# Performance work log

Hardware: AMD Instinct MI355X
Metric: run time of the kernel (lower is better)

Reference implementation:

```python
import jax, jax.numpy as jnp
import numpy as np

NUM_EMBEDDINGS = 512
EMBEDDING_DIM = 64
DECAY = 0.995
EXPECTED_COUNT = 1024 * 16 * 16 / NUM_EMBEDDINGS  # batch_size * H * W / K = 512.0


def setup_inputs() -> dict:
    key = jax.random.key(0)
    k1, k2 = jax.random.split(key)
    z_e = jax.random.normal(k1, (1024, EMBEDDING_DIM, 16, 16), dtype=jnp.float32)
    e = jax.random.normal(k2, (NUM_EMBEDDINGS, EMBEDDING_DIM), dtype=jnp.float32)
    N = jnp.ones((NUM_EMBEDDINGS,), dtype=jnp.float32) * EXPECTED_COUNT
    return {"z_e": z_e, "e": e, "N": N}


def reference(z_e, e, N):
    B, D, H, W = z_e.shape
    # (B, D, H, W) -> (B*H*W, D)
    z_flat = jnp.transpose(z_e, (0, 2, 3, 1)).reshape(-1, D)
    # squared euclidean distances: ||z||^2 + ||e||^2 - 2 z.e^T  -> [B*H*W, K]
    dist = (
        jnp.sum(z_flat * z_flat, axis=1, keepdims=True)
        + jnp.sum(e * e, axis=1)[None, :]
        - 2.0 * (z_flat @ e.T)
    )
    indices_flat = jnp.argmin(dist, axis=1)
    # embedding gather, back to (B, D, H, W)
    z_q = e[indices_flat].reshape(B, H, W, D)
    z_q = jnp.transpose(z_q, (0, 3, 1, 2))
    # training-mode EMA bincount update of cluster counts
    n_i = jnp.zeros((e.shape[0],), dtype=jnp.float32).at[indices_flat].add(1.0)
    N_new = DECAY * N + (1.0 - DECAY) * n_i
    return z_q, N_new
```

## Files before the change

kernel.cpp:

```cpp
#include <hip/hip_runtime.h>

#define KCODES 512
#define DIM    64
#define PXB    512
#define NCT    32

typedef __attribute__((ext_vector_type(8))) short  short8;
typedef __attribute__((ext_vector_type(4))) float  floatx4;

__device__ inline unsigned short f2bf(float x) {
    unsigned u = __float_as_uint(x);
    return (unsigned short)((u + 0x7FFFu + ((u >> 16) & 1u)) >> 16);
}
__device__ inline float bf2f(unsigned short h) { return __uint_as_float(((unsigned)h) << 16); }

__global__ __launch_bounds__(256) void vq_setup(const float* __restrict__ e,
        float* __restrict__ enorm, unsigned short* __restrict__ ehs,
        unsigned short* __restrict__ els, float* __restrict__ counts,
        unsigned* __restrict__ tick)
{
    const int tg = blockIdx.x * 256 + threadIdx.x;
    const int c = tg >> 6, j = tg & 63;
    const int p = j >> 3, i = j & 7;
    const int dsrc = ((p ^ (c & 7)) << 3) | i;
    float x = -2.f * e[c * DIM + dsrc];
    unsigned short h = f2bf(x);
    ehs[tg] = h;
    els[tg] = f2bf(x - bf2f(h));
    if (tg < KCODES) {
        const float* er = e + tg * DIM;
        float s = 0.f;
        #pragma unroll
        for (int d = 0; d < DIM; ++d) s = fmaf(er[d], er[d], s);
        enorm[tg]  = s;
        counts[tg] = 0.f;
        if (tg == 0) *tick = 0u;
    }
}

__global__ __launch_bounds__(1024) void vq_main(
        const float* __restrict__ z, const float* __restrict__ e,
        const unsigned short* __restrict__ ehs, const unsigned short* __restrict__ els,
        const float* __restrict__ enorm, const float* __restrict__ N,
        float* __restrict__ zq, float* __restrict__ counts,
        unsigned* __restrict__ tick, float* __restrict__ outN)
{
    __shared__ __align__(16) unsigned short eHs[KCODES * DIM];
    __shared__ __align__(16) unsigned short eLs[KCODES * DIM];
    __shared__ float ens[KCODES];
    __shared__ int   hist[KCODES];
    __shared__ int   idxs[PXB];
    __shared__ int   lastflag;

    const int t    = threadIdx.x;
    const int b    = blockIdx.x;
    const int lane = t & 63;
    const int wave = t >> 6;
    const int n16  = lane & 15;
    const int g4   = lane >> 4;

    {
        const short8* sh = (const short8*)ehs;
        const short8* sl = (const short8*)els;
        short8* dh = (short8*)eHs;
        short8* dl = (short8*)eLs;
        #pragma unroll
        for (int k = 0; k < 4; ++k) {
            dh[t + k * 1024] = sh[t + k * 1024];
            dl[t + k * 1024] = sl[t + k * 1024];
        }
        if (t < KCODES) { ens[t] = enorm[t]; hist[t] = 0; }
    }

    const int gp0 = b * PXB + wave * 32;
    short8 Ah[2][2], Al[2][2];
    #pragma unroll
    for (int pt = 0; pt < 2; ++pt) {
        const int gp = gp0 + pt * 16 + n16;
        const int bb = gp >> 8, hw = gp & 255;
        const float* zb = z + (size_t)bb * (DIM * 256) + hw;
        #pragma unroll
        for (int ks = 0; ks < 2; ++ks) {
            float v[8];
            #pragma unroll
            for (int q = 0; q < 8; ++q)
                v[q] = zb[(size_t)(ks * 32 + g4 * 8 + q) * 256];
            short8 hi, lo;
            #pragma unroll
            for (int q = 0; q < 8; ++q) {
                unsigned short h = f2bf(v[q]);
                hi[q] = (short)h;
                lo[q] = (short)f2bf(v[q] - bf2f(h));
            }
            Ah[pt][ks] = hi; Al[pt][ks] = lo;
        }
    }

    __syncthreads();

    const int xr = n16 & 7;
    const int byte_ks0 = n16 * 128 + (((g4    ) ^ xr) << 4);
    const int byte_ks1 = n16 * 128 + (((4 | g4) ^ xr) << 4);
    const char* hb = (const char*)eHs;
    const char* lb = (const char*)eLs;

    float bestv[2][4];
    int   bct[2][4];
    #pragma unroll
    for (int pt = 0; pt < 2; ++pt)
        #pragma unroll
        for (int r = 0; r < 4; ++r) { bestv[pt][r] = 3.4e38f; bct[pt][r] = 0; }

    #pragma unroll 4
    for (int ct = 0; ct < NCT; ++ct) {
        const int cb = ct * 2048;
        short8 Bh0 = *(const short8*)(hb + cb + byte_ks0);
        short8 Bh1 = *(const short8*)(hb + cb + byte_ks1);
        short8 Bl0 = *(const short8*)(lb + cb + byte_ks0);
        short8 Bl1 = *(const short8*)(lb + cb + byte_ks1);
        const float en = ens[ct * 16 + n16];
        #pragma unroll
        for (int pt = 0; pt < 2; ++pt) {
            floatx4 C = {en, en, en, en};
            C = __builtin_amdgcn_mfma_f32_16x16x32_bf16(Ah[pt][0], Bl0, C, 0, 0, 0);
            C = __builtin_amdgcn_mfma_f32_16x16x32_bf16(Ah[pt][1], Bl1, C, 0, 0, 0);
            C = __builtin_amdgcn_mfma_f32_16x16x32_bf16(Al[pt][0], Bh0, C, 0, 0, 0);
            C = __builtin_amdgcn_mfma_f32_16x16x32_bf16(Al[pt][1], Bh1, C, 0, 0, 0);
            C = __builtin_amdgcn_mfma_f32_16x16x32_bf16(Ah[pt][0], Bh0, C, 0, 0, 0);
            C = __builtin_amdgcn_mfma_f32_16x16x32_bf16(Ah[pt][1], Bh1, C, 0, 0, 0);
            #pragma unroll
            for (int r = 0; r < 4; ++r) {
                float s = C[r];
                if (s < bestv[pt][r]) { bestv[pt][r] = s; bct[pt][r] = ct; }
            }
        }
    }

    #pragma unroll
    for (int pt = 0; pt < 2; ++pt)
        #pragma unroll
        for (int r = 0; r < 4; ++r) {
            float v  = bestv[pt][r];
            int   id = bct[pt][r] * 16 + n16;
            #pragma unroll
            for (int off = 1; off < 16; off <<= 1) {
                float v1 = __shfl_xor(v, off, 16);
                int   i1 = __shfl_xor(id, off, 16);
                if (v1 < v || (v1 == v && i1 < id)) { v = v1; id = i1; }
            }
            if (n16 == 0) {
                const int px = wave * 32 + pt * 16 + g4 * 4 + r;
                idxs[px] = id;
                atomicAdd(&hist[id], 1);
            }
        }

    __syncthreads();

    {
        const int px = t & 511, dh = (t >> 9) * 32;
        const int bi = idxs[px];
        const int gp = b * PXB + px;
        const int bb = gp >> 8, hw = gp & 255;
        const float4* er4 = (const float4*)(e + bi * DIM + dh);
        float* ob = zq + (size_t)bb * (DIM * 256) + (size_t)dh * 256 + hw;
        #pragma unroll
        for (int q = 0; q < 8; ++q) {
            float4 v = er4[q];
            ob[(size_t)(4 * q + 0) * 256] = v.x;
            ob[(size_t)(4 * q + 1) * 256] = v.y;
            ob[(size_t)(4 * q + 2) * 256] = v.z;
            ob[(size_t)(4 * q + 3) * 256] = v.w;
        }
    }

    if (t < KCODES) { int h = hist[t]; if (h) atomicAdd(&counts[t], (float)h); }

    __syncthreads();
    if (t == 0) {
        __threadfence();
        unsigned o = __hip_atomic_fetch_add(tick, 1u, __ATOMIC_ACQ_REL,
                                            __HIP_MEMORY_SCOPE_AGENT);
        lastflag = (o == gridDim.x - 1u);
    }
    __syncthreads();
    if (lastflag && t < KCODES) {
        float c = __hip_atomic_load(&counts[t], __ATOMIC_RELAXED,
                                    __HIP_MEMORY_SCOPE_AGENT);
        outN[t] = 0.995f * N[t] + 0.005f * c;
    }
}

extern "C" void kernel_launch(void* const* d_in, const int* in_sizes, int n_in,
                              void* d_out, int out_size, void* d_ws, size_t ws_size,
                              hipStream_t stream) {
    const float* z = (const float*)d_in[0];
    const float* e = (const float*)d_in[1];
    const float* N = (const float*)d_in[2];
    float* out = (float*)d_out;
    const int nz     = in_sizes[0];
    const int npix   = nz / DIM;
    const int blocks = npix / PXB;

    char* ws = (char*)d_ws;
    float*          enorm  = (float*)(ws);
    float*          counts = (float*)(ws + 2048);
    unsigned*       tick   = (unsigned*)(ws + 4096);
    unsigned short* ehs    = (unsigned short*)(ws + 4352);
    unsigned short* els    = (unsigned short*)(ws + 4352 + KCODES * DIM * 2);

    vq_setup<<<(KCODES * DIM) / 256, 256, 0, stream>>>(e, enorm, ehs, els, counts, tick);
    vq_main<<<blocks, 1024, 0, stream>>>(z, e, ehs, els, enorm, N, out, counts,
                                         tick, out + nz);
}
```

Baseline: 202.2 us.

## Use single-pass fp16 MFMA distances with fp32 refinement of near-tie candidates

Replaces the split bf16 hi/lo three-product MFMA scheme with a single fp16 MFMA pass, which cuts the MFMA count per tile from six to two and halves LDS codebook traffic and footprint. A second shuffle reduction tracks the runner-up code. When the runner-up is within a fixed margin of the best, the pixel's two candidates are rescored exactly in fp32 from global memory. The histogram and count-flush ordering are moved to after this refinement. The risk is argmin mismatches if fp16 error exceeds the margin, plus extra work in the refinement pass.

```diff
diff --git a/kernel.cpp b/kernel.cpp
--- a/kernel.cpp
+++ b/kernel.cpp
@@ -4,29 +4,21 @@
 #define DIM    64
 #define PXB    512
 #define NCT    32
-
-typedef __attribute__((ext_vector_type(8))) short  short8;
-typedef __attribute__((ext_vector_type(4))) float  floatx4;
-
-__device__ inline unsigned short f2bf(float x) {
-    unsigned u = __float_as_uint(x);
-    return (unsigned short)((u + 0x7FFFu + ((u >> 16) & 1u)) >> 16);
-}
-__device__ inline float bf2f(unsigned short h) { return __uint_as_float(((unsigned)h) << 16); }
+#define MARGIN 0.125f
+
+typedef __attribute__((ext_vector_type(8))) short    short8;
+typedef __attribute__((ext_vector_type(8))) _Float16 half8;
+typedef __attribute__((ext_vector_type(4))) float    floatx4;
 
 __global__ __launch_bounds__(256) void vq_setup(const float* __restrict__ e,
-        float* __restrict__ enorm, unsigned short* __restrict__ ehs,
-        unsigned short* __restrict__ els, float* __restrict__ counts,
-        unsigned* __restrict__ tick)
+        float* __restrict__ enorm, _Float16* __restrict__ ehf,
+        float* __restrict__ counts, unsigned* __restrict__ tick)
 {
     const int tg = blockIdx.x * 256 + threadIdx.x;
     const int c = tg >> 6, j = tg & 63;
     const int p = j >> 3, i = j & 7;
     const int dsrc = ((p ^ (c & 7)) << 3) | i;
-    float x = -2.f * e[c * DIM + dsrc];
-    unsigned short h = f2bf(x);
-    ehs[tg] = h;
-    els[tg] = f2bf(x - bf2f(h));
+    ehf[tg] = (_Float16)(-2.f * e[c * DIM + dsrc]);
     if (tg < KCODES) {
         const float* er = e + tg * DIM;
         float s = 0.f;
@@ -38,18 +30,18 @@
     }
 }
 
-__global__ __launch_bounds__(1024) void vq_main(
+__global__ __launch_bounds__(1024, 8) void vq_main(
         const float* __restrict__ z, const float* __restrict__ e,
-        const unsigned short* __restrict__ ehs, const unsigned short* __restrict__ els,
-        const float* __restrict__ enorm, const float* __restrict__ N,
-        float* __restrict__ zq, float* __restrict__ counts,
-        unsigned* __restrict__ tick, float* __restrict__ outN)
+        const _Float16* __restrict__ ehf, const float* __restrict__ enorm,
+        const float* __restrict__ N, float* __restrict__ zq,
+        float* __restrict__ counts, unsigned* __restrict__ tick,
+        float* __restrict__ outN)
 {
-    __shared__ __align__(16) unsigned short eHs[KCODES * DIM];
-    __shared__ __align__(16) unsigned short eLs[KCODES * DIM];
+    __shared__ __align__(16) _Float16 eHs[KCODES * DIM];
     __shared__ float ens[KCODES];
     __shared__ int   hist[KCODES];
     __shared__ int   idxs[PXB];
+    __shared__ int   ref2[PXB];
     __shared__ int   lastflag;
 
     const int t    = threadIdx.x;
@@ -60,20 +52,16 @@
     const int g4   = lane >> 4;
 
     {
-        const short8* sh = (const short8*)ehs;
-        const short8* sl = (const short8*)els;
-        short8* dh = (short8*)eHs;
-        short8* dl = (short8*)eLs;
-        #pragma unroll
-        for (int k = 0; k < 4; ++k) {
-            dh[t + k * 1024] = sh[t + k * 1024];
-            dl[t + k * 1024] = sl[t + k * 1024];
-        }
+        const short8* src = (const short8*)ehf;
+        short8* dst = (short8*)eHs;
+        #pragma unroll
+        for (int k = 0; k < 4; ++k)
+            dst[t + k * 1024] = src[t + k * 1024];
         if (t < KCODES) { ens[t] = enorm[t]; hist[t] = 0; }
     }
 
     const int gp0 = b * PXB + wave * 32;
-    short8 Ah[2][2], Al[2][2];
+    half8 A[2][2];
     #pragma unroll
     for (int pt = 0; pt < 2; ++pt) {
         const int gp = gp0 + pt * 16 + n16;
@@ -85,24 +73,19 @@
             #pragma unroll
             for (int q = 0; q < 8; ++q)
                 v[q] = zb[(size_t)(ks * 32 + g4 * 8 + q) * 256];
-            short8 hi, lo;
-            #pragma unroll
-            for (int q = 0; q < 8; ++q) {
-                unsigned short h = f2bf(v[q]);
-                hi[q] = (short)h;
-                lo[q] = (short)f2bf(v[q] - bf2f(h));
-            }
-            Ah[pt][ks] = hi; Al[pt][ks] = lo;
+            half8 h;
+            #pragma unroll
+            for (int q = 0; q < 8; ++q) h[q] = (_Float16)v[q];
+            A[pt][ks] = h;
         }
     }
 
     __syncthreads();
 
     const int xr = n16 & 7;
-    const int byte_ks0 = n16 * 128 + (((g4    ) ^ xr) << 4);
-    const int byte_ks1 = n16 * 128 + (((4 | g4) ^ xr) << 4);
+    const int byte0 = n16 * 128 + (((g4    ) ^ xr) << 4);
+    const int byte1 = n16 * 128 + (((4 | g4) ^ xr) << 4);
     const char* hb = (const char*)eHs;
-    const char* lb = (const char*)eLs;
 
     float bestv[2][4];
     int   bct[2][4];
@@ -111,23 +94,17 @@
         #pragma unroll
         for (int r = 0; r < 4; ++r) { bestv[pt][r] = 3.4e38f; bct[pt][r] = 0; }
 
-    #pragma unroll 4
+    #pragma unroll 2
     for (int ct = 0; ct < NCT; ++ct) {
         const int cb = ct * 2048;
-        short8 Bh0 = *(const short8*)(hb + cb + byte_ks0);
-        short8 Bh1 = *(const short8*)(hb + cb + byte_ks1);
-        short8 Bl0 = *(const short8*)(lb + cb + byte_ks0);
-        short8 Bl1 = *(const short8*)(lb + cb + byte_ks1);
+        half8 B0 = *(const half8*)(hb + cb + byte0);
+        half8 B1 = *(const half8*)(hb + cb + byte1);
         const float en = ens[ct * 16 + n16];
         #pragma unroll
         for (int pt = 0; pt < 2; ++pt) {
             floatx4 C = {en, en, en, en};
-            C = __builtin_amdgcn_mfma_f32_16x16x32_bf16(Ah[pt][0], Bl0, C, 0, 0, 0);
-            C = __builtin_amdgcn_mfma_f32_16x16x32_bf16(Ah[pt][1], Bl1, C, 0, 0, 0);
-            C = __builtin_amdgcn_mfma_f32_16x16x32_bf16(Al[pt][0], Bh0, C, 0, 0, 0);
-            C = __builtin_amdgcn_mfma_f32_16x16x32_bf16(Al[pt][1], Bh1, C, 0, 0, 0);
-            C = __builtin_amdgcn_mfma_f32_16x16x32_bf16(Ah[pt][0], Bh0, C, 0, 0, 0);
-            C = __builtin_amdgcn_mfma_f32_16x16x32_bf16(Ah[pt][1], Bh1, C, 0, 0, 0);
+            C = __builtin_amdgcn_mfma_f32_16x16x32_f16(A[pt][0], B0, C, 0, 0, 0);
+            C = __builtin_amdgcn_mfma_f32_16x16x32_f16(A[pt][1], B1, C, 0, 0, 0);
             #pragma unroll
             for (int r = 0; r < 4; ++r) {
                 float s = C[r];
@@ -140,21 +117,66 @@
     for (int pt = 0; pt < 2; ++pt)
         #pragma unroll
         for (int r = 0; r < 4; ++r) {
-            float v  = bestv[pt][r];
-            int   id = bct[pt][r] * 16 + n16;
+            const float v1 = bestv[pt][r];
+            const int   i1 = bct[pt][r] * 16 + n16;
+            float v = v1; int i = i1;
             #pragma unroll
             for (int off = 1; off < 16; off <<= 1) {
-                float v1 = __shfl_xor(v, off, 16);
-                int   i1 = __shfl_xor(id, off, 16);
-                if (v1 < v || (v1 == v && i1 < id)) { v = v1; id = i1; }
+                float vs = __shfl_xor(v, off, 16);
+                int   is = __shfl_xor(i, off, 16);
+                if (vs < v || (vs == v && is < i)) { v = vs; i = is; }
+            }
+            float w  = (i1 == i) ? 3.4e38f : v1;
+            int   wi = i1;
+            #pragma unroll
+            for (int off = 1; off < 16; off <<= 1) {
+                float vs = __shfl_xor(w, off, 16);
+                int   is = __shfl_xor(wi, off, 16);
+                if (vs < w || (vs == w && is < wi)) { w = vs; wi = is; }
             }
             if (n16 == 0) {
                 const int px = wave * 32 + pt * 16 + g4 * 4 + r;
-                idxs[px] = id;
-                atomicAdd(&hist[id], 1);
-            }
-        }
-
+                idxs[px] = i;
+                ref2[px] = (w - v < MARGIN) ? wi : -1;
+            }
+        }
+
+    __syncthreads();
+
+    if (t < PXB) {
+        int bi = idxs[t];
+        const int r2 = ref2[t];
+        if (r2 >= 0) {
+            const int gp = b * PXB + t;
+            const int bb = gp >> 8, hw = gp & 255;
+            const float* zb = z + (size_t)bb * (DIM * 256) + hw;
+            const float* e1 = e + bi * DIM;
+            const float* e2 = e + r2 * DIM;
+            float d1 = 0.f, d2 = 0.f;
+            #pragma unroll
+            for (int d = 0; d < DIM; ++d) {
+                const float zd = zb[(size_t)d * 256];
+                d1 = fmaf(zd, e1[d], d1);
+                d2 = fmaf(zd, e2[d], d2);
+            }
+            const float s1 = fmaf(-2.f, d1, ens[bi]);
+            const float s2 = fmaf(-2.f, d2, ens[r2]);
+            if (s2 < s1 || (s2 == s1 && r2 < bi)) bi = r2;
+            idxs[t] = bi;
+        }
+        atomicAdd(&hist[bi], 1);
+    }
+
+    __syncthreads();
+
+    if (t < KCODES) { int h = hist[t]; if (h) atomicAdd(&counts[t], (float)h); }
+    __syncthreads();
+    if (t == 0) {
+        __threadfence();
+        unsigned o = __hip_atomic_fetch_add(tick, 1u, __ATOMIC_ACQ_REL,
+                                            __HIP_MEMORY_SCOPE_AGENT);
+        lastflag = (o == gridDim.x - 1u);
+    }
     __syncthreads();
 
     {
@@ -174,16 +196,6 @@
         }
     }
 
-    if (t < KCODES) { int h = hist[t]; if (h) atomicAdd(&counts[t], (float)h); }
-
-    __syncthreads();
-    if (t == 0) {
-        __threadfence();
-        unsigned o = __hip_atomic_fetch_add(tick, 1u, __ATOMIC_ACQ_REL,
-                                            __HIP_MEMORY_SCOPE_AGENT);
-        lastflag = (o == gridDim.x - 1u);
-    }
-    __syncthreads();
     if (lastflag && t < KCODES) {
         float c = __hip_atomic_load(&counts[t], __ATOMIC_RELAXED,
                                     __HIP_MEMORY_SCOPE_AGENT);
@@ -203,13 +215,12 @@
     const int blocks = npix / PXB;
 
     char* ws = (char*)d_ws;
-    float*          enorm  = (float*)(ws);
-    float*          counts = (float*)(ws + 2048);
-    unsigned*       tick   = (unsigned*)(ws + 4096);
-    unsigned short* ehs    = (unsigned short*)(ws + 4352);
-    unsigned short* els    = (unsigned short*)(ws + 4352 + KCODES * DIM * 2);
-
-    vq_setup<<<(KCODES * DIM) / 256, 256, 0, stream>>>(e, enorm, ehs, els, counts, tick);
-    vq_main<<<blocks, 1024, 0, stream>>>(z, e, ehs, els, enorm, N, out, counts,
+    float*     enorm  = (float*)(ws);
+    float*     counts = (float*)(ws + 2048);
+    unsigned*  tick   = (unsigned*)(ws + 4096);
+    _Float16*  ehf    = (_Float16*)(ws + 4352);
+
+    vq_setup<<<(KCODES * DIM) / 256, 256, 0, stream>>>(e, enorm, ehf, counts, tick);
+    vq_main<<<blocks, 1024, 0, stream>>>(z, e, ehf, enorm, N, out, counts,
                                          tick, out + nz);
 }
```

Measured after the change: 171.7 us. 1.18x faster.
